# Performance work log

Hardware: AMD Instinct MI355X
Metric: run time of the kernel (lower is better)

Reference implementation:

```python
import jax, jax.numpy as jnp
import numpy as np

NUM_CLUSTERS = 128
C = NUM_CLUSTERS + 1  # bincount minlength = number_clusters + 1
SOFTMAX_TEMP = 1.0


def setup_inputs() -> dict:
    key = jax.random.key(0)
    k1, k2, k3, k4 = jax.random.split(key, 4)
    B, N, D = 32, 4096, 64
    Bc = 4  # clusters batch dim; heads = B // Bc = 8
    return {
        "queries": jax.random.normal(k1, (B, N, D), dtype=jnp.float32),
        "keys": jax.random.normal(k2, (B, N, D), dtype=jnp.float32),
        "values": jax.random.normal(k3, (B, N, D), dtype=jnp.float32),
        "clusters": jax.random.randint(k4, (Bc, N), 0, C).astype(jnp.int64),
    }


def _segment_sum_batched(x, groups, num_segments):
    # x: [B, N, D], groups: [B, N] -> [B, num_segments, D]
    return jax.vmap(lambda xb, gb: jax.ops.segment_sum(xb, gb, num_segments=num_segments))(x, groups)


def reference(queries, keys, values, clusters):
    B, N, D = queries.shape
    Bc = clusters.shape[0]
    rep = B // Bc
    g = clusters.astype(jnp.int32)
    # per-cluster counts (bincount with minlength=C)
    counts = jax.vmap(lambda gb: jax.ops.segment_sum(jnp.ones((N,), jnp.float32), gb, num_segments=C))(g)
    # repeat assignments/counts across heads: torch .repeat(rep, 1) == tile on dim 0
    groups = jnp.tile(g, (rep, 1))          # [B, N]
    counts = jnp.tile(counts, (rep, 1))     # [B, C]
    w = jnp.where(counts > 0, 1.0 / counts, 0.0)  # 1/counts (guard empty clusters)

    Q_center = _segment_sum_batched(queries, groups, C) * w[..., None]  # [B, C, D]
    K_center = _segment_sum_batched(keys, groups, C) * w[..., None]
    V_center = _segment_sum_batched(values, groups, C) * w[..., None]

    QK = jnp.einsum('bqd,bkd->bqk', Q_center, K_center)  # [B, C, C]
    A = jax.nn.softmax(SOFTMAX_TEMP * QK, axis=-1)
    # weighted softmax: reweight by key-cluster counts, renormalize
    A = A * counts[:, None, :]
    A_full = A / A.sum(axis=-1, keepdims=True)

    V = jnp.einsum('bqk,bkd->bqd', A_full, V_center)  # [B, C, D]
    # Broadcast centers back to all cluster members (gather)
    out = jnp.take_along_axis(V, groups[..., None], axis=1)  # [B, N, D]
    return out, A_full[:, :, 0]
```

## Files before the change

### kernel.cpp

```cpp
#include <hip/hip_runtime.h>

#define B_ 32
#define N_ 4096
#define D_ 64
#define C_ 129
#define BC_ 4
#define CG_ 33
#define QROWS_ 8

__global__ __launch_bounds__(1024) void k_sort(const int* __restrict__ cl,
                                               float* __restrict__ counts,
                                               int* __restrict__ offsets,
                                               int* __restrict__ sidx) {
    __shared__ int cnt[C_];
    __shared__ int base[C_];
    __shared__ int cur[C_];
    int bc = blockIdx.x, tid = threadIdx.x;
    for (int i = tid; i < C_; i += 1024) { cnt[i] = 0; cur[i] = 0; }
    __syncthreads();
    const int4* g4 = (const int4*)(cl + bc * N_);
    for (int n = tid; n < N_ / 4; n += 1024) {
        int4 c4 = g4[n];
        atomicAdd(&cnt[c4.x], 1);
        atomicAdd(&cnt[c4.y], 1);
        atomicAdd(&cnt[c4.z], 1);
        atomicAdd(&cnt[c4.w], 1);
    }
    __syncthreads();
    if (tid < C_) {
        int acc = 0;
        for (int i = 0; i < tid; i++) acc += cnt[i];
        base[tid] = acc;
    }
    __syncthreads();
    for (int i = tid; i < C_; i += 1024) {
        counts[bc * C_ + i] = (float)cnt[i];
        offsets[bc * (C_ + 1) + i] = base[i];
    }
    if (tid == 0) offsets[bc * (C_ + 1) + C_] = N_;
    for (int n = tid; n < N_ / 4; n += 1024) {
        int4 c4 = g4[n];
        int n0 = n * 4;
        sidx[bc * N_ + base[c4.x] + atomicAdd(&cur[c4.x], 1)] = n0;
        sidx[bc * N_ + base[c4.y] + atomicAdd(&cur[c4.y], 1)] = n0 + 1;
        sidx[bc * N_ + base[c4.z] + atomicAdd(&cur[c4.z], 1)] = n0 + 2;
        sidx[bc * N_ + base[c4.w] + atomicAdd(&cur[c4.w], 1)] = n0 + 3;
    }
}

__global__ __launch_bounds__(256) void k_segsum4(const float* __restrict__ q,
                                                 const float* __restrict__ k,
                                                 const float* __restrict__ v,
                                                 const int* __restrict__ offsets,
                                                 const int* __restrict__ sidx,
                                                 float* __restrict__ sums) {
    int bid = blockIdx.x;
    int cg = bid % CG_;
    int b = bid / CG_;
    int wave = threadIdx.x >> 6, lane = threadIdx.x & 63;
    int c = cg * 4 + wave;
    if (c >= C_) return;
    int bc = b & 3;
    int start = offsets[bc * (C_ + 1) + c];
    int end = offsets[bc * (C_ + 1) + c + 1];
    int cnt = end - start;
    int sub = lane >> 4, d4 = lane & 15;

    const float4* q4 = (const float4*)(q + (size_t)b * N_ * D_);
    const float4* k4 = (const float4*)(k + (size_t)b * N_ * D_);
    const float4* v4 = (const float4*)(v + (size_t)b * N_ * D_);
    const int* si = sidx + bc * N_;

    float4 aq = make_float4(0.f, 0.f, 0.f, 0.f);
    float4 ak = make_float4(0.f, 0.f, 0.f, 0.f);
    float4 av = make_float4(0.f, 0.f, 0.f, 0.f);

    if (cnt > 0) {
        int last = end - 1;
        int ia = start + sub, ib = ia + 4, ic = ia + 8, id = ia + 12;
        int ra = si[min(ia, last)], rb = si[min(ib, last)];
        int rc = si[min(ic, last)], rd = si[min(id, last)];
        for (int i0 = start; i0 < end; i0 += 16) {
            int ca = ia, cb = ib, cc = ic, cd = id;
            int ua = ra, ub = rb, uc = rc, ud = rd;
            ia += 16; ib += 16; ic += 16; id += 16;
            if (i0 + 16 < end) {
                ra = si[min(ia, last)]; rb = si[min(ib, last)];
                rc = si[min(ic, last)]; rd = si[min(id, last)];
            }
            float ma = (ca < end) ? 1.f : 0.f;
            float mb = (cb < end) ? 1.f : 0.f;
            float mc = (cc < end) ? 1.f : 0.f;
            float md = (cd < end) ? 1.f : 0.f;
            float4 qa = q4[ua * 16 + d4], qb = q4[ub * 16 + d4];
            float4 qc = q4[uc * 16 + d4], qd = q4[ud * 16 + d4];
            float4 ka = k4[ua * 16 + d4], kb = k4[ub * 16 + d4];
            float4 kc = k4[uc * 16 + d4], kd = k4[ud * 16 + d4];
            float4 va = v4[ua * 16 + d4], vb = v4[ub * 16 + d4];
            float4 vc = v4[uc * 16 + d4], vd = v4[ud * 16 + d4];
            aq.x += ma * qa.x + mb * qb.x + mc * qc.x + md * qd.x;
            aq.y += ma * qa.y + mb * qb.y + mc * qc.y + md * qd.y;
            aq.z += ma * qa.z + mb * qb.z + mc * qc.z + md * qd.z;
            aq.w += ma * qa.w + mb * qb.w + mc * qc.w + md * qd.w;
            ak.x += ma * ka.x + mb * kb.x + mc * kc.x + md * kd.x;
            ak.y += ma * ka.y + mb * kb.y + mc * kc.y + md * kd.y;
            ak.z += ma * ka.z + mb * kb.z + mc * kc.z + md * kd.z;
            ak.w += ma * ka.w + mb * kb.w + mc * kc.w + md * kd.w;
            av.x += ma * va.x + mb * vb.x + mc * vc.x + md * vd.x;
            av.y += ma * va.y + mb * vb.y + mc * vc.y + md * vd.y;
            av.z += ma * va.z + mb * vb.z + mc * vc.z + md * vd.z;
            av.w += ma * va.w + mb * vb.w + mc * vc.w + md * vd.w;
        }
    }
#pragma unroll
    for (int off = 16; off <= 32; off <<= 1) {
        aq.x += __shfl_xor(aq.x, off, 64); aq.y += __shfl_xor(aq.y, off, 64);
        aq.z += __shfl_xor(aq.z, off, 64); aq.w += __shfl_xor(aq.w, off, 64);
        ak.x += __shfl_xor(ak.x, off, 64); ak.y += __shfl_xor(ak.y, off, 64);
        ak.z += __shfl_xor(ak.z, off, 64); ak.w += __shfl_xor(ak.w, off, 64);
        av.x += __shfl_xor(av.x, off, 64); av.y += __shfl_xor(av.y, off, 64);
        av.z += __shfl_xor(av.z, off, 64); av.w += __shfl_xor(av.w, off, 64);
    }
    if (sub == 0) {
        float w = (cnt > 0) ? 1.f / (float)cnt : 0.f;
        float4 oq = make_float4(aq.x * w, aq.y * w, aq.z * w, aq.w * w);
        float4 ok = make_float4(ak.x * w, ak.y * w, ak.z * w, ak.w * w);
        float4 ov = make_float4(av.x * w, av.y * w, av.z * w, av.w * w);
        ((float4*)(sums + (size_t)b * C_ * D_))[c * 16 + d4] = oq;
        ((float4*)(sums + ((size_t)B_ + b) * C_ * D_))[c * 16 + d4] = ok;
        ((float4*)(sums + ((size_t)2 * B_ + b) * C_ * D_))[c * 16 + d4] = ov;
    }
}

__global__ __launch_bounds__(256, 2) void k_attn_sc(const float* __restrict__ sums,
                                                    const float* __restrict__ counts,
                                                    const int* __restrict__ offsets,
                                                    const int* __restrict__ sidx,
                                                    float* __restrict__ out,
                                                    float* __restrict__ aout) {
    __shared__ float4 kc4[C_ * 17];
    __shared__ float4 vc4[C_ * 17];
    __shared__ float cnt_s[C_];
    __shared__ float arow[4][2][132];

    int bid = blockIdx.x;
    int b = bid & 31;
    int qg = bid >> 5;
    int q0 = qg * QROWS_;
    int qcnt = min(QROWS_, C_ - q0);
    int tid = threadIdx.x;
    int bc = b & 3;

    for (int i = tid; i < C_; i += 256)
        cnt_s[i] = counts[bc * C_ + i];

    const float4* qsum4 = (const float4*)(sums + (size_t)b * C_ * D_);
    const float4* ksum4 = (const float4*)(sums + ((size_t)B_ + b) * C_ * D_);
    const float4* vsum4 = (const float4*)(sums + ((size_t)2 * B_ + b) * C_ * D_);

    for (int i = tid; i < C_ * 16; i += 256) {
        int c = i >> 4, d4 = i & 15;
        kc4[c * 17 + d4] = ksum4[i];
        vc4[c * 17 + d4] = vsum4[i];
    }
    __syncthreads();

    const int* si = sidx + bc * N_;
    float4* ob = (float4*)(out + (size_t)b * N_ * D_);

    int wave = __builtin_amdgcn_readfirstlane(tid >> 6);
    int lane = tid & 63;

    for (int tt = wave; tt * 2 < qcnt; tt += 4) {
        int t2 = tt * 2;
        const float4* qp0 = qsum4 + (size_t)(q0 + min(t2 + 0, qcnt - 1)) * 16;
        const float4* qp1 = qsum4 + (size_t)(q0 + min(t2 + 1, qcnt - 1)) * 16;
        float s0[2] = {0, 0}, s1[2] = {0, 0}, s2[2] = {0, 0};
#pragma unroll 4
        for (int d4 = 0; d4 < 16; d4++) {
            float4 kv0 = kc4[lane * 17 + d4];
            float4 kv1 = kc4[(lane + 64) * 17 + d4];
            float4 kv2 = kc4[128 * 17 + d4];
            float4 qv0 = qp0[d4], qv1 = qp1[d4];
            s0[0] += qv0.x * kv0.x + qv0.y * kv0.y + qv0.z * kv0.z + qv0.w * kv0.w;
            s1[0] += qv0.x * kv1.x + qv0.y * kv1.y + qv0.z * kv1.z + qv0.w * kv1.w;
            s2[0] += qv0.x * kv2.x + qv0.y * kv2.y + qv0.z * kv2.z + qv0.w * kv2.w;
            s0[1] += qv1.x * kv0.x + qv1.y * kv0.y + qv1.z * kv0.z + qv1.w * kv0.w;
            s1[1] += qv1.x * kv1.x + qv1.y * kv1.y + qv1.z * kv1.z + qv1.w * kv1.w;
            s2[1] += qv1.x * kv2.x + qv1.y * kv2.y + qv1.z * kv2.z + qv1.w * kv2.w;
        }
#pragma unroll
        for (int r = 0; r < 2; r++) {
            if (t2 + r >= qcnt) break;
            int qrow = q0 + t2 + r;
            float m = fmaxf(s0[r], s1[r]);
            if (lane == 0) m = fmaxf(m, s2[r]);
            for (int off = 32; off > 0; off >>= 1)
                m = fmaxf(m, __shfl_xor(m, off, 64));
            float e0 = __expf(s0[r] - m) * cnt_s[lane];
            float e1 = __expf(s1[r] - m) * cnt_s[lane + 64];
            float e2 = (lane == 0) ? __expf(s2[r] - m) * cnt_s[128] : 0.f;
            float sum = e0 + e1 + e2;
            for (int off = 32; off > 0; off >>= 1)
                sum += __shfl_xor(sum, off, 64);
            float inv = 1.f / sum;
            float a0 = e0 * inv, a1 = e1 * inv;
            arow[wave][r][lane] = a0;
            arow[wave][r][64 + lane] = a1;
            if (lane == 0) {
                arow[wave][r][128] = e2 * inv;
                aout[b * C_ + qrow] = a0;
            }
        }
        __builtin_amdgcn_s_waitcnt(0);
        __builtin_amdgcn_sched_barrier(0);
        int rr = lane >> 5;
        int half = (lane >> 4) & 1;
        int d4 = lane & 15;
        const float4* ar4 = (const float4*)arow[wave][rr];
        float4 o = make_float4(0.f, 0.f, 0.f, 0.f);
        int k4base = half * 16;
        for (int k4 = k4base; k4 < k4base + 16; k4++) {
            float4 a4 = ar4[k4];
            float4 v0 = vc4[(k4 * 4 + 0) * 17 + d4];
            float4 v1 = vc4[(k4 * 4 + 1) * 17 + d4];
            float4 v2 = vc4[(k4 * 4 + 2) * 17 + d4];
            float4 v3 = vc4[(k4 * 4 + 3) * 17 + d4];
            o.x += a4.x * v0.x + a4.y * v1.x + a4.z * v2.x + a4.w * v3.x;
            o.y += a4.x * v0.y + a4.y * v1.y + a4.z * v2.y + a4.w * v3.y;
            o.z += a4.x * v0.z + a4.y * v1.z + a4.z * v2.z + a4.w * v3.z;
            o.w += a4.x * v0.w + a4.y * v1.w + a4.z * v2.w + a4.w * v3.w;
        }
        o.x += __shfl_xor(o.x, 16, 64);
        o.y += __shfl_xor(o.y, 16, 64);
        o.z += __shfl_xor(o.z, 16, 64);
        o.w += __shfl_xor(o.w, 16, 64);
        {
            float a128 = arow[wave][rr][128];
            float4 vv = vc4[128 * 17 + d4];
            o.x += a128 * vv.x; o.y += a128 * vv.y;
            o.z += a128 * vv.z; o.w += a128 * vv.w;
        }
        if (t2 + rr < qcnt) {
            int qrow = q0 + t2 + rr;
            int s = offsets[bc * (C_ + 1) + qrow];
            int e = offsets[bc * (C_ + 1) + qrow + 1];
            for (int mm = s + half; mm < e; mm += 2) {
                int n = si[mm];
                ob[n * 16 + d4] = o;
            }
        }
    }
}

extern "C" void kernel_launch(void* const* d_in, const int* in_sizes, int n_in,
                              void* d_out, int out_size, void* d_ws, size_t ws_size,
                              hipStream_t stream) {
    const float* q = (const float*)d_in[0];
    const float* k = (const float*)d_in[1];
    const float* v = (const float*)d_in[2];
    const int* cl = (const int*)d_in[3];
    float* out = (float*)d_out;
    float* aout = out + (size_t)B_ * N_ * D_;

    float* ws = (float*)d_ws;
    float* counts = ws;
    float* sums = ws + 1024;
    int* offsets = (int*)(sums + (size_t)3 * B_ * C_ * D_);
    int* sidx = offsets + 4 * (C_ + 1);

    k_sort<<<BC_, 1024, 0, stream>>>(cl, counts, offsets, sidx);
    k_segsum4<<<B_ * CG_, 256, 0, stream>>>(q, k, v, offsets, sidx, sums);
    k_attn_sc<<<17 * B_, 256, 0, stream>>>(sums, counts, offsets, sidx, out, aout);
}
```

Before: 164.7 us.

## Replace gathered segment sum with streaming LDS-atomic partial sums

The sorted-index gather segment-sum kernel is replaced by a streaming kernel. Each block reads a contiguous chunk of rows of one of q/k/v and accumulates per-cluster sums in shared memory with LDS atomics. Partial sums go to a workspace, and the last-arriving block per tensor/batch (tracked with a global atomic counter) reduces all chunks and applies the 1/count scaling. This targets the scattered gather reads of the old kernel, at the cost of shared-memory atomic contention, about 33KB of LDS per block, and extra partial-sum traffic.

```diff
diff --git a/kernel.cpp b/kernel.cpp
--- a/kernel.cpp
+++ b/kernel.cpp
@@ -5,17 +5,21 @@
 #define D_ 64
 #define C_ 129
 #define BC_ 4
-#define CG_ 33
+#define CD_ (C_ * D_)
+#define NCH_ 8
+#define CHROWS_ (N_ / NCH_)
 #define QROWS_ 8
 
 __global__ __launch_bounds__(1024) void k_sort(const int* __restrict__ cl,
                                                float* __restrict__ counts,
                                                int* __restrict__ offsets,
-                                               int* __restrict__ sidx) {
+                                               int* __restrict__ sidx,
+                                               int* __restrict__ pcnt) {
     __shared__ int cnt[C_];
     __shared__ int base[C_];
     __shared__ int cur[C_];
     int bc = blockIdx.x, tid = threadIdx.x;
+    if (bc == 0 && tid < 96) pcnt[tid] = 0;
     for (int i = tid; i < C_; i += 1024) { cnt[i] = 0; cur[i] = 0; }
     __syncthreads();
     const int4* g4 = (const int4*)(cl + bc * N_);
@@ -48,87 +52,85 @@
     }
 }
 
-__global__ __launch_bounds__(256) void k_segsum4(const float* __restrict__ q,
-                                                 const float* __restrict__ k,
-                                                 const float* __restrict__ v,
-                                                 const int* __restrict__ offsets,
-                                                 const int* __restrict__ sidx,
-                                                 float* __restrict__ sums) {
+__global__ __launch_bounds__(256) void k_segsum_stream(const float* __restrict__ q,
+                                                       const float* __restrict__ k,
+                                                       const float* __restrict__ v,
+                                                       const int* __restrict__ cl,
+                                                       const float* __restrict__ counts,
+                                                       float* __restrict__ part,
+                                                       int* __restrict__ pcnt,
+                                                       float* __restrict__ sums) {
+    __shared__ float acc[CD_];
+    __shared__ int cl_s[CHROWS_];
+    __shared__ int lastflag;
     int bid = blockIdx.x;
-    int cg = bid % CG_;
-    int b = bid / CG_;
-    int wave = threadIdx.x >> 6, lane = threadIdx.x & 63;
-    int c = cg * 4 + wave;
-    if (c >= C_) return;
+    int tb = bid % 96;
+    int chunk = bid / 96;
+    int t = tb >> 5;
+    int b = tb & 31;
     int bc = b & 3;
-    int start = offsets[bc * (C_ + 1) + c];
-    int end = offsets[bc * (C_ + 1) + c + 1];
-    int cnt = end - start;
-    int sub = lane >> 4, d4 = lane & 15;
-
-    const float4* q4 = (const float4*)(q + (size_t)b * N_ * D_);
-    const float4* k4 = (const float4*)(k + (size_t)b * N_ * D_);
-    const float4* v4 = (const float4*)(v + (size_t)b * N_ * D_);
-    const int* si = sidx + bc * N_;
-
-    float4 aq = make_float4(0.f, 0.f, 0.f, 0.f);
-    float4 ak = make_float4(0.f, 0.f, 0.f, 0.f);
-    float4 av = make_float4(0.f, 0.f, 0.f, 0.f);
-
-    if (cnt > 0) {
-        int last = end - 1;
-        int ia = start + sub, ib = ia + 4, ic = ia + 8, id = ia + 12;
-        int ra = si[min(ia, last)], rb = si[min(ib, last)];
-        int rc = si[min(ic, last)], rd = si[min(id, last)];
-        for (int i0 = start; i0 < end; i0 += 16) {
-            int ca = ia, cb = ib, cc = ic, cd = id;
-            int ua = ra, ub = rb, uc = rc, ud = rd;
-            ia += 16; ib += 16; ic += 16; id += 16;
-            if (i0 + 16 < end) {
-                ra = si[min(ia, last)]; rb = si[min(ib, last)];
-                rc = si[min(ic, last)]; rd = si[min(id, last)];
+    int tid = threadIdx.x;
+    const float* x = (t == 0) ? q : (t == 1) ? k : v;
+
+    for (int i = tid; i < CD_; i += 256) acc[i] = 0.f;
+    int n0 = chunk * CHROWS_;
+    for (int i = tid; i < CHROWS_; i += 256) cl_s[i] = cl[bc * N_ + n0 + i];
+    __syncthreads();
+
+    const float4* x4 = (const float4*)(x + (size_t)b * N_ * D_) + (size_t)n0 * 16;
+    int g = tid >> 4, d4 = tid & 15;
+    for (int r0 = 0; r0 < CHROWS_; r0 += 128) {
+        float4 xv0 = x4[(r0 + 0 * 16 + g) * 16 + d4];
+        float4 xv1 = x4[(r0 + 1 * 16 + g) * 16 + d4];
+        float4 xv2 = x4[(r0 + 2 * 16 + g) * 16 + d4];
+        float4 xv3 = x4[(r0 + 3 * 16 + g) * 16 + d4];
+        float4 xv4 = x4[(r0 + 4 * 16 + g) * 16 + d4];
+        float4 xv5 = x4[(r0 + 5 * 16 + g) * 16 + d4];
+        float4 xv6 = x4[(r0 + 6 * 16 + g) * 16 + d4];
+        float4 xv7 = x4[(r0 + 7 * 16 + g) * 16 + d4];
+        int c0 = cl_s[r0 + 0 * 16 + g], c1 = cl_s[r0 + 1 * 16 + g];
+        int c2 = cl_s[r0 + 2 * 16 + g], c3 = cl_s[r0 + 3 * 16 + g];
+        int c4_ = cl_s[r0 + 4 * 16 + g], c5 = cl_s[r0 + 5 * 16 + g];
+        int c6 = cl_s[r0 + 6 * 16 + g], c7 = cl_s[r0 + 7 * 16 + g];
+#define ACC1(cc, xv)                                            \
+        {   float* pa = &acc[(cc) * 64 + d4 * 4];               \
+            atomicAdd(pa + 0, (xv).x); atomicAdd(pa + 1, (xv).y); \
+            atomicAdd(pa + 2, (xv).z); atomicAdd(pa + 3, (xv).w); }
+        ACC1(c0, xv0) ACC1(c1, xv1) ACC1(c2, xv2) ACC1(c3, xv3)
+        ACC1(c4_, xv4) ACC1(c5, xv5) ACC1(c6, xv6) ACC1(c7, xv7)
+#undef ACC1
+    }
+    __syncthreads();
+
+    float4* my = (float4*)(part + ((size_t)tb * NCH_ + chunk) * CD_);
+    const float4* accf4 = (const float4*)acc;
+    for (int i = tid; i < CD_ / 4; i += 256) my[i] = accf4[i];
+
+    __threadfence();
+    if (tid == 0) {
+        int old = __hip_atomic_fetch_add(&pcnt[tb], 1, __ATOMIC_ACQ_REL,
+                                         __HIP_MEMORY_SCOPE_AGENT);
+        lastflag = (old == NCH_ - 1);
+    }
+    __syncthreads();
+    if (lastflag) {
+        __threadfence();
+        const float4* pt = (const float4*)(part + (size_t)tb * NCH_ * CD_);
+        float4* dst = (float4*)(sums + (size_t)tb * CD_);
+        for (int i = tid; i < CD_ / 4; i += 256) {
+            float4 s = accf4[i];
+#pragma unroll
+            for (int ch = 0; ch < NCH_; ch++) {
+                if (ch == chunk) continue;
+                float4 p = pt[ch * (CD_ / 4) + i];
+                s.x += p.x; s.y += p.y; s.z += p.z; s.w += p.w;
             }
-            float ma = (ca < end) ? 1.f : 0.f;
-            float mb = (cb < end) ? 1.f : 0.f;
-            float mc = (cc < end) ? 1.f : 0.f;
-            float md = (cd < end) ? 1.f : 0.f;
-            float4 qa = q4[ua * 16 + d4], qb = q4[ub * 16 + d4];
-            float4 qc = q4[uc * 16 + d4], qd = q4[ud * 16 + d4];
-            float4 ka = k4[ua * 16 + d4], kb = k4[ub * 16 + d4];
-            float4 kc = k4[uc * 16 + d4], kd = k4[ud * 16 + d4];
-            float4 va = v4[ua * 16 + d4], vb = v4[ub * 16 + d4];
-            float4 vc = v4[uc * 16 + d4], vd = v4[ud * 16 + d4];
-            aq.x += ma * qa.x + mb * qb.x + mc * qc.x + md * qd.x;
-            aq.y += ma * qa.y + mb * qb.y + mc * qc.y + md * qd.y;
-            aq.z += ma * qa.z + mb * qb.z + mc * qc.z + md * qd.z;
-            aq.w += ma * qa.w + mb * qb.w + mc * qc.w + md * qd.w;
-            ak.x += ma * ka.x + mb * kb.x + mc * kc.x + md * kd.x;
-            ak.y += ma * ka.y + mb * kb.y + mc * kc.y + md * kd.y;
-            ak.z += ma * ka.z + mb * kb.z + mc * kc.z + md * kd.z;
-            ak.w += ma * ka.w + mb * kb.w + mc * kc.w + md * kd.w;
-            av.x += ma * va.x + mb * vb.x + mc * vc.x + md * vd.x;
-            av.y += ma * va.y + mb * vb.y + mc * vc.y + md * vd.y;
-            av.z += ma * va.z + mb * vb.z + mc * vc.z + md * vd.z;
-            av.w += ma * va.w + mb * vb.w + mc * vc.w + md * vd.w;
-        }
-    }
-#pragma unroll
-    for (int off = 16; off <= 32; off <<= 1) {
-        aq.x += __shfl_xor(aq.x, off, 64); aq.y += __shfl_xor(aq.y, off, 64);
-        aq.z += __shfl_xor(aq.z, off, 64); aq.w += __shfl_xor(aq.w, off, 64);
-        ak.x += __shfl_xor(ak.x, off, 64); ak.y += __shfl_xor(ak.y, off, 64);
-        ak.z += __shfl_xor(ak.z, off, 64); ak.w += __shfl_xor(ak.w, off, 64);
-        av.x += __shfl_xor(av.x, off, 64); av.y += __shfl_xor(av.y, off, 64);
-        av.z += __shfl_xor(av.z, off, 64); av.w += __shfl_xor(av.w, off, 64);
-    }
-    if (sub == 0) {
-        float w = (cnt > 0) ? 1.f / (float)cnt : 0.f;
-        float4 oq = make_float4(aq.x * w, aq.y * w, aq.z * w, aq.w * w);
-        float4 ok = make_float4(ak.x * w, ak.y * w, ak.z * w, ak.w * w);
-        float4 ov = make_float4(av.x * w, av.y * w, av.z * w, av.w * w);
-        ((float4*)(sums + (size_t)b * C_ * D_))[c * 16 + d4] = oq;
-        ((float4*)(sums + ((size_t)B_ + b) * C_ * D_))[c * 16 + d4] = ok;
-        ((float4*)(sums + ((size_t)2 * B_ + b) * C_ * D_))[c * 16 + d4] = ov;
+            int c = i >> 4;
+            float cnt = counts[bc * C_ + c];
+            float w = (cnt > 0.f) ? 1.f / cnt : 0.f;
+            s.x *= w; s.y *= w; s.z *= w; s.w *= w;
+            dst[i] = s;
+        }
     }
 }
 
@@ -266,10 +268,12 @@
     float* ws = (float*)d_ws;
     float* counts = ws;
     float* sums = ws + 1024;
-    int* offsets = (int*)(sums + (size_t)3 * B_ * C_ * D_);
+    float* part = sums + (size_t)3 * B_ * CD_;
+    int* pcnt = (int*)(part + (size_t)96 * NCH_ * CD_);
+    int* offsets = pcnt + 256;
     int* sidx = offsets + 4 * (C_ + 1);
 
-    k_sort<<<BC_, 1024, 0, stream>>>(cl, counts, offsets, sidx);
-    k_segsum4<<<B_ * CG_, 256, 0, stream>>>(q, k, v, offsets, sidx, sums);
+    k_sort<<<BC_, 1024, 0, stream>>>(cl, counts, offsets, sidx, pcnt);
+    k_segsum_stream<<<NCH_ * 96, 256, 0, stream>>>(q, k, v, cl, counts, part, pcnt, sums);
     k_attn_sc<<<17 * B_, 256, 0, stream>>>(sums, counts, offsets, sidx, out, aout);
 }
```

Measured after the change: 361.4 us. 119% more time.
